# Performance work log

Hardware: AMD Instinct MI355X
Metric: run time of the kernel (lower is better)

Reference implementation:

```python
import jax, jax.numpy as jnp
import numpy as np

B, L = 2048, 120            # batch, sentence length
V, P = 114042, 102          # word vocab, position vocab
WE, PE = 50, 5              # word / position embedding dims
F, K, R = 230, 3, 53        # filters, kernel size, relations
D = WE + 2 * PE             # feature dim = 60


def setup_inputs() -> dict:
    key = jax.random.key(0)
    ks = jax.random.split(key, 10)
    sent = jax.random.randint(ks[0], (B, L), 0, V)
    pf = jax.random.randint(ks[1], (B, 2, L), 0, P)
    # entity positions: ensure 1 <= pool0 < pool1 <= L-1 so all 3 segments are non-empty
    p0 = jax.random.randint(ks[2], (B,), 3, 40)
    p1 = jax.random.randint(ks[3], (B,), 60, 115)
    epos = jnp.stack([p0, p1], axis=1) - 1  # forward uses pool = epos + 1
    s = 0.02
    W_word = jax.random.normal(ks[4], (V, WE), jnp.float32) * s
    W_pos1 = jax.random.normal(ks[5], (P, PE), jnp.float32) * s
    W_pos2 = jax.random.normal(ks[6], (P, PE), jnp.float32) * s
    conv_w = jax.random.normal(ks[7], (F, 1, K, D), jnp.float32) * s
    conv_b = jnp.zeros((F,), jnp.float32)
    lin_w = jax.random.normal(ks[8], (R, 3 * F), jnp.float32) * s
    lin_b = jnp.zeros((R,), jnp.float32)
    return dict(sent=sent, pf=pf, epos=epos, W_word=W_word, W_pos1=W_pos1,
                W_pos2=W_pos2, conv_w=conv_w, conv_b=conv_b, lin_w=lin_w, lin_b=lin_b)


def reference(sent, pf, epos, W_word, W_pos1, W_pos2, conv_w, conv_b, lin_w, lin_b):
    # embeddings -> [B, L, D]
    emb = jnp.concatenate([W_word[sent], W_pos1[pf[:, 0]], W_pos2[pf[:, 1]]], axis=-1)
    # conv over (length, feature) with full-width kernel; dropout is identity (eval)
    x = emb[:, None, :, :]  # [B, 1, L, D]
    y = jax.lax.conv_general_dilated(x, conv_w, window_strides=(1, 1),
                                     padding=[(K // 2, K // 2), (0, 0)])  # [B, F, L, 1]
    y = jnp.tanh(y[..., 0] + conv_b[None, :, None])  # [B, F, L]
    # piecewise (3-segment) max pooling, segment boundaries per batch item
    pool = epos + 1                                   # [B, 2]
    pos = jnp.arange(L)[None, :]                      # [1, L]
    seg = (pos >= pool[:, :1]).astype(jnp.int32) + (pos >= pool[:, 1:]).astype(jnp.int32)  # [B, L] in {0,1,2}
    neg = jnp.finfo(y.dtype).min
    pooled = [jnp.max(jnp.where((seg == s)[:, None, :], y, neg), axis=2) for s in range(3)]
    feats = jnp.stack(pooled, axis=-1).reshape(B, F * 3)  # matches torch cat+view ordering
    return feats @ lin_w.T + lin_b  # [B, R]
```

## Files before the change

### kernel.cpp

```cpp
#include <hip/hip_runtime.h>
#include <math.h>

#define BB 2048
#define LL 120
#define WE_ 50
#define PE_ 5
#define DD 60
#define FF 230
#define KK 3
#define RR 53

#define NKT 6
#define NNT 15
#define NPAD 240
#define EMB_ELEMS 7936

#define WS_BP    0
#define WS_LT    92160
#define WS_EMBG  246784

#define ACC_BIAS 16.0f

typedef __attribute__((ext_vector_type(8))) short short8_t;
typedef __attribute__((ext_vector_type(4))) short short4_t;
typedef __attribute__((ext_vector_type(4))) float float4_t;

__device__ __forceinline__ unsigned f2bf(float x) {
    unsigned u = __builtin_bit_cast(unsigned, x);
    return (u + 0x7fffu + ((u >> 16) & 1u)) >> 16;
}

__device__ __forceinline__ float tanh_fast(float x) {
    float t = __expf(2.0f * x);
    return 1.0f - 2.0f * __builtin_amdgcn_rcpf(t + 1.0f);
}

__global__ __launch_bounds__(256) void pcnn_prep_b(const float* __restrict__ convw,
                                                   unsigned short* __restrict__ bp) {
    int idx = blockIdx.x * 256 + threadIdx.x;
    if (idx >= NNT * NKT * 64 * 8) return;
    int j    = idx & 7;
    int lane = (idx >> 3) & 63;
    int t    = idx >> 9;
    int kt   = t % NKT;
    int nt   = t / NKT;
    int f    = nt * 16 + (lane & 15);
    int klin = kt * 32 + (lane >> 4) * 8 + j;
    float v = (f < FF && klin < KK * DD) ? convw[f * (KK * DD) + klin] : 0.0f;
    bp[idx] = (unsigned short)f2bf(v);
}

__global__ __launch_bounds__(256) void pcnn_prep_lt(const float* __restrict__ linw,
                                                    float* __restrict__ lt) {
    int idx = blockIdx.x * 256 + threadIdx.x;
    if (idx >= 690 * 56) return;
    int i = idx / 56;
    int r = idx - i * 56;
    lt[idx] = (r < RR) ? linw[r * (3 * FF) + i] : 0.0f;
}

__global__ __launch_bounds__(256) void pcnn_gather(
    const int* __restrict__ sent, const int* __restrict__ pf,
    const float* __restrict__ Wword, const float* __restrict__ Wpos1,
    const float* __restrict__ Wpos2, unsigned* __restrict__ embg32)
{
    int idx = blockIdx.x * 256 + threadIdx.x;
    if (idx >= BB * LL * 30) return;
    int c  = idx % 30;
    int lc = idx / 30;
    int l  = lc % LL;
    int b  = lc / LL;
    unsigned pk;
    if (c < 25) {
        int w = sent[b * LL + l];
        float2 v = *(const float2*)(Wword + w * WE_ + 2 * c);
        pk = f2bf(v.x) | (f2bf(v.y) << 16);
    } else {
        int p = pf[b * 2 * LL + l];
        int q = pf[b * 2 * LL + LL + l];
        int j0 = (c - 25) * 2, j1 = j0 + 1;
        float f0 = (j0 < PE_) ? Wpos1[p * PE_ + j0] : Wpos2[q * PE_ + j0 - PE_];
        float f1 = (j1 < PE_) ? Wpos1[p * PE_ + j1] : Wpos2[q * PE_ + j1 - PE_];
        pk = f2bf(f0) | (f2bf(f1) << 16);
    }
    embg32[idx] = pk;
}

__global__ __launch_bounds__(256) void pcnn_mfma(
    const int* __restrict__ epos,
    const unsigned short* __restrict__ embg,
    const unsigned short* __restrict__ bp, const float* __restrict__ convb,
    const float* __restrict__ linw_t, const float* __restrict__ linb,
    float* __restrict__ out)
{
    __shared__ __align__(16) union SM {
        unsigned short emb[EMB_ELEMS];
        float pool[4 * NPAD * 3 + NPAD * 3 + 4 * 56];
    } sm;
    unsigned* const keys  = (unsigned*)sm.pool;
    float* const feats    = sm.pool + 4 * NPAD * 3;
    float* const part2    = sm.pool + 4 * NPAD * 3 + NPAD * 3;

    const int b    = blockIdx.x;
    const int tid  = threadIdx.x;
    const int wid  = tid >> 6;
    const int lane = tid & 63;

    const int pool0 = epos[b * 2 + 0] + 1;
    const int pool1 = epos[b * 2 + 1] + 1;

    {
        unsigned* e32 = (unsigned*)sm.emb;
        for (int i = tid; i < 32 + 336; i += 256) {
            int d = (i < 32) ? i : (3600 + i);
            e32[d] = 0u;
        }
    }
    {
        const unsigned short* eb = embg + (size_t)b * (LL * DD);
        #pragma unroll
        for (int k = 0; k < 4; ++k) {
            int c = tid + k * 256;
            if (c < 900) {
                float4 v = *(const float4*)(eb + c * 8);
                *(float4*)((char*)sm.emb + 128 + c * 16) = v;
            }
        }
    }
    __syncthreads();

    short8_t afrag[2][NKT];
    #pragma unroll
    for (int tm2 = 0; tm2 < 2; ++tm2) {
        int l = (2 * wid + tm2) * 16 + (lane & 15);
        #pragma unroll
        for (int kt = 0; kt < NKT; ++kt) {
            int e = l * DD + 4 + kt * 32 + (lane >> 4) * 8;
            short4_t lo = *(const short4_t*)(sm.emb + e);
            short4_t hi = *(const short4_t*)(sm.emb + e + 4);
            short8_t f8;
            f8[0] = lo[0]; f8[1] = lo[1]; f8[2] = lo[2]; f8[3] = lo[3];
            f8[4] = hi[0]; f8[5] = hi[1]; f8[6] = hi[2]; f8[7] = hi[3];
            afrag[tm2][kt] = f8;
        }
    }
    __syncthreads();

    for (int i = tid; i < NPAD * 3; i += 256) keys[i] = 0u;

    const int qrow = (lane >> 4) * 4;
    const int fcol = lane & 15;
    int off[2][4];
    #pragma unroll
    for (int tm2 = 0; tm2 < 2; ++tm2) {
        #pragma unroll
        for (int r = 0; r < 4; ++r) {
            int l = wid * 32 + tm2 * 16 + qrow + r;
            int seg = (l >= pool0) + (l >= pool1);
            off[tm2][r] = fcol * 3 + seg;
        }
    }
    const bool skip_hi = (wid == 3) && (lane >= 32);
    __syncthreads();

    #pragma unroll 3
    for (int nt = 0; nt < NNT; ++nt) {
        const short8_t* bpv = (const short8_t*)(bp) + (nt * NKT) * 64;
        short8_t bfrag[NKT];
        #pragma unroll
        for (int kt = 0; kt < NKT; ++kt) bfrag[kt] = bpv[kt * 64 + lane];

        float4_t acc0 = {0.f, 0.f, 0.f, 0.f};
        float4_t acc1 = {0.f, 0.f, 0.f, 0.f};
        #pragma unroll
        for (int kt = 0; kt < NKT; ++kt) {
            acc0 = __builtin_amdgcn_mfma_f32_16x16x32_bf16(afrag[0][kt], bfrag[kt], acc0, 0, 0, 0);
            acc1 = __builtin_amdgcn_mfma_f32_16x16x32_bf16(afrag[1][kt], bfrag[kt], acc1, 0, 0, 0);
        }

        unsigned* kb = keys + nt * 48;
        #pragma unroll
        for (int r = 0; r < 4; ++r)
            atomicMax(&kb[off[0][r]], __builtin_bit_cast(unsigned, acc0[r] + ACC_BIAS));
        if (!skip_hi) {
            #pragma unroll
            for (int r = 0; r < 4; ++r)
                atomicMax(&kb[off[1][r]], __builtin_bit_cast(unsigned, acc1[r] + ACC_BIAS));
        }
    }
    __syncthreads();

    for (int i = tid; i < FF * 3; i += 256) {
        float m = __builtin_bit_cast(float, keys[i]) - ACC_BIAS;
        int f = i / 3;
        feats[i] = tanh_fast(m + convb[f]);
    }
    __syncthreads();

    {
        int i0 = (690 * wid) >> 2;
        int i1 = (690 * (wid + 1)) >> 2;
        float acc = 0.0f;
        if (lane < 56) {
            #pragma unroll 4
            for (int i = i0; i < i1; ++i)
                acc += feats[i] * linw_t[i * 56 + lane];
            part2[wid * 56 + lane] = acc;
        }
    }
    __syncthreads();
    if (tid < RR) {
        float s = part2[tid] + part2[56 + tid] + part2[112 + tid] + part2[168 + tid];
        out[b * RR + tid] = s + linb[tid];
    }
}

extern "C" void kernel_launch(void* const* d_in, const int* in_sizes, int n_in,
                              void* d_out, int out_size, void* d_ws, size_t ws_size,
                              hipStream_t stream) {
    const int*   sent  = (const int*)d_in[0];
    const int*   pf    = (const int*)d_in[1];
    const int*   epos  = (const int*)d_in[2];
    const float* Wword = (const float*)d_in[3];
    const float* Wpos1 = (const float*)d_in[4];
    const float* Wpos2 = (const float*)d_in[5];
    const float* convw = (const float*)d_in[6];
    const float* convb = (const float*)d_in[7];
    const float* linw  = (const float*)d_in[8];
    const float* linb  = (const float*)d_in[9];
    float* out = (float*)d_out;

    char* ws = (char*)d_ws;
    unsigned short* bp     = (unsigned short*)(ws + WS_BP);
    float*          linw_t = (float*)(ws + WS_LT);
    unsigned short* embg   = (unsigned short*)(ws + WS_EMBG);

    pcnn_prep_b<<<(NNT * NKT * 64 * 8 + 255) / 256, 256, 0, stream>>>(convw, bp);
    pcnn_prep_lt<<<(690 * 56 + 255) / 256, 256, 0, stream>>>(linw, linw_t);
    pcnn_gather<<<(BB * LL * 30) / 256, 256, 0, stream>>>(sent, pf, Wword, Wpos1, Wpos2,
                                                          (unsigned*)embg);
    pcnn_mfma<<<BB, 256, 0, stream>>>(epos, embg, bp, convb, linw_t, linb, out);
}
```

Before: 166.5 us.

## Merge prep and gather kernels, prefetch B fragments, pre-reduce uniform-segment atomics

Folds the two weight-prep kernels and the embedding gather into one launch, using block-index ranges to pick the role, which removes two kernel launches and their inter-kernel gaps. In the MFMA kernel the B fragments for the next filter tile are loaded while the current tile computes, double-buffered in registers. When all four rows a lane holds fall in the same pooling segment, the lane takes their max and issues one LDS atomicMax instead of four. The register prefetch raises VGPR pressure and may reduce occupancy.

```diff
diff --git a/kernel.cpp b/kernel.cpp
--- a/kernel.cpp
+++ b/kernel.cpp
@@ -21,6 +21,12 @@
 
 #define ACC_BIAS 16.0f
 
+#define GATHER_ITEMS (BB * LL * 30)
+#define GATHER_BLKS  (GATHER_ITEMS / 256)
+#define BP_ITEMS     (NNT * NKT * 64 * 8)
+#define LT_ITEMS     (690 * 56)
+#define PREP_BLKS    ((BP_ITEMS + LT_ITEMS + 255) / 256)
+
 typedef __attribute__((ext_vector_type(8))) short short8_t;
 typedef __attribute__((ext_vector_type(4))) short short4_t;
 typedef __attribute__((ext_vector_type(4))) float float4_t;
@@ -35,55 +41,54 @@
     return 1.0f - 2.0f * __builtin_amdgcn_rcpf(t + 1.0f);
 }
 
-__global__ __launch_bounds__(256) void pcnn_prep_b(const float* __restrict__ convw,
-                                                   unsigned short* __restrict__ bp) {
-    int idx = blockIdx.x * 256 + threadIdx.x;
-    if (idx >= NNT * NKT * 64 * 8) return;
-    int j    = idx & 7;
-    int lane = (idx >> 3) & 63;
-    int t    = idx >> 9;
-    int kt   = t % NKT;
-    int nt   = t / NKT;
-    int f    = nt * 16 + (lane & 15);
-    int klin = kt * 32 + (lane >> 4) * 8 + j;
-    float v = (f < FF && klin < KK * DD) ? convw[f * (KK * DD) + klin] : 0.0f;
-    bp[idx] = (unsigned short)f2bf(v);
-}
-
-__global__ __launch_bounds__(256) void pcnn_prep_lt(const float* __restrict__ linw,
-                                                    float* __restrict__ lt) {
-    int idx = blockIdx.x * 256 + threadIdx.x;
-    if (idx >= 690 * 56) return;
-    int i = idx / 56;
-    int r = idx - i * 56;
-    lt[idx] = (r < RR) ? linw[r * (3 * FF) + i] : 0.0f;
-}
-
-__global__ __launch_bounds__(256) void pcnn_gather(
+__global__ __launch_bounds__(256) void pcnn_gp(
     const int* __restrict__ sent, const int* __restrict__ pf,
     const float* __restrict__ Wword, const float* __restrict__ Wpos1,
-    const float* __restrict__ Wpos2, unsigned* __restrict__ embg32)
+    const float* __restrict__ Wpos2, const float* __restrict__ convw,
+    const float* __restrict__ linw,
+    unsigned* __restrict__ embg32, unsigned short* __restrict__ bp,
+    float* __restrict__ lt)
 {
-    int idx = blockIdx.x * 256 + threadIdx.x;
-    if (idx >= BB * LL * 30) return;
-    int c  = idx % 30;
-    int lc = idx / 30;
-    int l  = lc % LL;
-    int b  = lc / LL;
-    unsigned pk;
-    if (c < 25) {
-        int w = sent[b * LL + l];
-        float2 v = *(const float2*)(Wword + w * WE_ + 2 * c);
-        pk = f2bf(v.x) | (f2bf(v.y) << 16);
+    int bid = blockIdx.x;
+    if (bid < GATHER_BLKS) {
+        int idx = bid * 256 + threadIdx.x;
+        int c  = idx % 30;
+        int lc = idx / 30;
+        int l  = lc % LL;
+        int b  = lc / LL;
+        unsigned pk;
+        if (c < 25) {
+            int w = sent[b * LL + l];
+            float2 v = *(const float2*)(Wword + w * WE_ + 2 * c);
+            pk = f2bf(v.x) | (f2bf(v.y) << 16);
+        } else {
+            int p = pf[b * 2 * LL + l];
+            int q = pf[b * 2 * LL + LL + l];
+            int j0 = (c - 25) * 2, j1 = j0 + 1;
+            float f0 = (j0 < PE_) ? Wpos1[p * PE_ + j0] : Wpos2[q * PE_ + j0 - PE_];
+            float f1 = (j1 < PE_) ? Wpos1[p * PE_ + j1] : Wpos2[q * PE_ + j1 - PE_];
+            pk = f2bf(f0) | (f2bf(f1) << 16);
+        }
+        embg32[idx] = pk;
     } else {
-        int p = pf[b * 2 * LL + l];
-        int q = pf[b * 2 * LL + LL + l];
-        int j0 = (c - 25) * 2, j1 = j0 + 1;
-        float f0 = (j0 < PE_) ? Wpos1[p * PE_ + j0] : Wpos2[q * PE_ + j0 - PE_];
-        float f1 = (j1 < PE_) ? Wpos1[p * PE_ + j1] : Wpos2[q * PE_ + j1 - PE_];
-        pk = f2bf(f0) | (f2bf(f1) << 16);
-    }
-    embg32[idx] = pk;
+        int idx = (bid - GATHER_BLKS) * 256 + threadIdx.x;
+        if (idx < BP_ITEMS) {
+            int j    = idx & 7;
+            int lane = (idx >> 3) & 63;
+            int t    = idx >> 9;
+            int kt   = t % NKT;
+            int nt   = t / NKT;
+            int f    = nt * 16 + (lane & 15);
+            int klin = kt * 32 + (lane >> 4) * 8 + j;
+            float v = (f < FF && klin < KK * DD) ? convw[f * (KK * DD) + klin] : 0.0f;
+            bp[idx] = (unsigned short)f2bf(v);
+        } else if (idx < BP_ITEMS + LT_ITEMS) {
+            int k = idx - BP_ITEMS;
+            int i = k / 56;
+            int r = k - i * 56;
+            lt[k] = (r < RR) ? linw[r * (3 * FF) + i] : 0.0f;
+        }
+    }
 }
 
 __global__ __launch_bounds__(256) void pcnn_mfma(
@@ -160,33 +165,53 @@
             off[tm2][r] = fcol * 3 + seg;
         }
     }
+    const bool same0 = (off[0][0] == off[0][3]);
+    const bool same1 = (off[1][0] == off[1][3]);
     const bool skip_hi = (wid == 3) && (lane >= 32);
     __syncthreads();
 
-    #pragma unroll 3
+    const short8_t* bpv = (const short8_t*)bp;
+    short8_t bA[NKT], bB[NKT];
+    #pragma unroll
+    for (int kt = 0; kt < NKT; ++kt) bA[kt] = bpv[kt * 64 + lane];
+
     for (int nt = 0; nt < NNT; ++nt) {
-        const short8_t* bpv = (const short8_t*)(bp) + (nt * NKT) * 64;
-        short8_t bfrag[NKT];
-        #pragma unroll
-        for (int kt = 0; kt < NKT; ++kt) bfrag[kt] = bpv[kt * 64 + lane];
+        if (nt + 1 < NNT) {
+            const short8_t* bn = bpv + (size_t)(nt + 1) * NKT * 64;
+            #pragma unroll
+            for (int kt = 0; kt < NKT; ++kt) bB[kt] = bn[kt * 64 + lane];
+        }
 
         float4_t acc0 = {0.f, 0.f, 0.f, 0.f};
         float4_t acc1 = {0.f, 0.f, 0.f, 0.f};
         #pragma unroll
         for (int kt = 0; kt < NKT; ++kt) {
-            acc0 = __builtin_amdgcn_mfma_f32_16x16x32_bf16(afrag[0][kt], bfrag[kt], acc0, 0, 0, 0);
-            acc1 = __builtin_amdgcn_mfma_f32_16x16x32_bf16(afrag[1][kt], bfrag[kt], acc1, 0, 0, 0);
+            acc0 = __builtin_amdgcn_mfma_f32_16x16x32_bf16(afrag[0][kt], bA[kt], acc0, 0, 0, 0);
+            acc1 = __builtin_amdgcn_mfma_f32_16x16x32_bf16(afrag[1][kt], bA[kt], acc1, 0, 0, 0);
         }
 
         unsigned* kb = keys + nt * 48;
-        #pragma unroll
-        for (int r = 0; r < 4; ++r)
-            atomicMax(&kb[off[0][r]], __builtin_bit_cast(unsigned, acc0[r] + ACC_BIAS));
-        if (!skip_hi) {
+        if (same0) {
+            float m = fmaxf(fmaxf(acc0[0], acc0[1]), fmaxf(acc0[2], acc0[3]));
+            atomicMax(&kb[off[0][0]], __builtin_bit_cast(unsigned, m + ACC_BIAS));
+        } else {
             #pragma unroll
             for (int r = 0; r < 4; ++r)
-                atomicMax(&kb[off[1][r]], __builtin_bit_cast(unsigned, acc1[r] + ACC_BIAS));
-        }
+                atomicMax(&kb[off[0][r]], __builtin_bit_cast(unsigned, acc0[r] + ACC_BIAS));
+        }
+        if (!skip_hi) {
+            if (same1) {
+                float m = fmaxf(fmaxf(acc1[0], acc1[1]), fmaxf(acc1[2], acc1[3]));
+                atomicMax(&kb[off[1][0]], __builtin_bit_cast(unsigned, m + ACC_BIAS));
+            } else {
+                #pragma unroll
+                for (int r = 0; r < 4; ++r)
+                    atomicMax(&kb[off[1][r]], __builtin_bit_cast(unsigned, acc1[r] + ACC_BIAS));
+            }
+        }
+
+        #pragma unroll
+        for (int kt = 0; kt < NKT; ++kt) bA[kt] = bB[kt];
     }
     __syncthreads();
 
@@ -235,9 +260,8 @@
     float*          linw_t = (float*)(ws + WS_LT);
     unsigned short* embg   = (unsigned short*)(ws + WS_EMBG);
 
-    pcnn_prep_b<<<(NNT * NKT * 64 * 8 + 255) / 256, 256, 0, stream>>>(convw, bp);
-    pcnn_prep_lt<<<(690 * 56 + 255) / 256, 256, 0, stream>>>(linw, linw_t);
-    pcnn_gather<<<(BB * LL * 30) / 256, 256, 0, stream>>>(sent, pf, Wword, Wpos1, Wpos2,
-                                                          (unsigned*)embg);
+    pcnn_gp<<<GATHER_BLKS + PREP_BLKS, 256, 0, stream>>>(
+        sent, pf, Wword, Wpos1, Wpos2, convw, linw,
+        (unsigned*)embg, bp, linw_t);
     pcnn_mfma<<<BB, 256, 0, stream>>>(epos, embg, bp, convb, linw_t, linb, out);
 }
```

New measurement: 165.6 us. No clear change (-0.5%).
